# Kernel optimization log

Hardware: AMD Instinct MI355X
Metric: run time of the kernel (lower is better)

## Reference

```python
import jax, jax.numpy as jnp
import numpy as np

VOCAB, E, H, L, N = 32000, 256, 512, 512, 64


def setup_inputs() -> dict:
    key = jax.random.key(0)
    ks = jax.random.split(key, 8)
    s_in = 1.0 / np.sqrt(H + E)
    return {
        "x": jax.random.randint(ks[0], (L, N), 0, VOCAB),
        "emb": jax.random.normal(ks[1], (VOCAB, E), dtype=jnp.float32),
        # weights stored (in, out); math identical to torch Linear with W.T
        "Wz": jax.random.uniform(ks[2], (H + E, H), jnp.float32, -s_in, s_in),
        "bz": jax.random.uniform(ks[3], (H,), jnp.float32, -s_in, s_in),
        "Wr": jax.random.uniform(ks[4], (H + E, H), jnp.float32, -s_in, s_in),
        "br": jax.random.uniform(ks[5], (H,), jnp.float32, -s_in, s_in),
        "Wh": jax.random.uniform(ks[6], (H + E, H), jnp.float32, -s_in, s_in),
        "bh": jax.random.uniform(ks[7], (H,), jnp.float32, -s_in, s_in),
    }


def reference(x, emb, Wz, bz, Wr, br, Wh, bh):
    # x: (L, N) int indices -> embedded once: (L, N, E)
    xe = emb[x]
    h0 = jnp.zeros((x.shape[1], Wz.shape[1]), dtype=emb.dtype)

    def step(h, e_t):
        hx = jnp.concatenate([h, e_t], axis=1)            # (N, H+E)
        z = jax.nn.sigmoid(hx @ Wz + bz)                  # update gate
        r = jax.nn.sigmoid(hx @ Wr + br)                  # reset gate
        rhx = jnp.concatenate([r * h, e_t], axis=1)
        h_tilde = jnp.tanh(rhx @ Wh + bh)
        h_new = (1.0 - z) * h + z * h_tilde
        return h_new, h_new

    _, hs = jax.lax.scan(step, h0, xe)                    # hs: (L, N, H)
    return hs
```

## Files before the change

### kernel.cpp

```cpp
#include <hip/hip_runtime.h>


#define LSTEPS 512
#define NBATCH 64
#define HDIM   512
#define EDIM   256
#define KDIM   768
#define NBLK   32
#define TPB    256

typedef _Float16 f16x8 __attribute__((ext_vector_type(8)));
typedef float    f32x4 __attribute__((ext_vector_type(4)));
typedef unsigned long long u64;

__device__ __forceinline__ float sigm(float x){ return 1.0f/(1.0f+__expf(-x)); }
__device__ __forceinline__ float tanh_fast(float x){
  float e = __expf(2.0f*x);
  return 1.0f - 2.0f/(e + 1.0f);
}
__device__ __forceinline__ unsigned f16b(float x){
  union { _Float16 h; unsigned short u; } c; c.h = (_Float16)x; return (unsigned)c.u;
}

__global__ void prep_w(const float* __restrict__ Wz, const float* __restrict__ Wr,
                       const float* __restrict__ Wh, _Float16* __restrict__ wbuf){
  int tid = blockIdx.x*256 + threadIdx.x;
  int g   = tid / (HDIM*KDIM);
  int rem = tid - g*(HDIM*KDIM);
  int j   = rem / KDIM;
  int k   = rem - j*KDIM;
  const float* W = (g==0) ? Wz : ((g==1) ? Wr : Wh);
  wbuf[tid] = (_Float16)W[(size_t)k*HDIM + j];
}

__global__ void prep_emb(const int* __restrict__ x, const float* __restrict__ emb,
                         _Float16* __restrict__ ebuf){
  int tid = blockIdx.x*256 + threadIdx.x;
  int k4  = tid & 63;
  int tn  = tid >> 6;
  int row = x[tn];
  const float4 v = *(const float4*)(emb + (size_t)row*EDIM + (k4<<2));
  union { _Float16 h[4]; uint2 u; } p;
  p.h[0] = (_Float16)v.x; p.h[1] = (_Float16)v.y;
  p.h[2] = (_Float16)v.z; p.h[3] = (_Float16)v.w;
  *(uint2*)(ebuf + (size_t)tn*EDIM + (k4<<2)) = p.u;
}

__device__ __forceinline__ void store_x(_Float16* buf, int jc2, int n0, int lane,
                                        float v0, float v1, float v2, float v3){
  unsigned p01 = f16b(v0) | (f16b(v1) << 16);
  unsigned p23 = f16b(v2) | (f16b(v3) << 16);
  unsigned q01 = __shfl_xor(p01, 1, 64);
  unsigned q23 = __shfl_xor(p23, 1, 64);
  unsigned w0, w1; int r0;
  if (lane & 1){
    w0 = (q23 & 0xffffu) | (p23 << 16);
    w1 = (q23 >> 16)     | (p23 & 0xffff0000u);
    r0 = n0 + 2;
  } else {
    w0 = (p01 & 0xffffu) | (q01 << 16);
    w1 = (p01 >> 16)     | (q01 & 0xffff0000u);
    r0 = n0;
  }
  __hip_atomic_store((unsigned*)(buf + (size_t)r0*HDIM + jc2),     w0,
                     __ATOMIC_RELAXED, __HIP_MEMORY_SCOPE_AGENT);
  __hip_atomic_store((unsigned*)(buf + (size_t)(r0+1)*HDIM + jc2), w1,
                     __ATOMIC_RELAXED, __HIP_MEMORY_SCOPE_AGENT);
}

__device__ __forceinline__ void waitfl(unsigned* fl, unsigned target){
  const int l31 = threadIdx.x & 31;
  for (;;){
    unsigned v = __hip_atomic_load(&fl[l31], __ATOMIC_RELAXED, __HIP_MEMORY_SCOPE_AGENT);
    if (__all(v >= target)) break;
  }
}

__global__ __launch_bounds__(TPB, 1) void gru_persist(
    const _Float16* __restrict__ wbuf,
    const _Float16* __restrict__ ebuf,
    const float* __restrict__ bz, const float* __restrict__ br, const float* __restrict__ bh,
    _Float16* __restrict__ hx,
    _Float16* __restrict__ rhx,
    unsigned* __restrict__ hfl,
    unsigned* __restrict__ rhfl,
    float* __restrict__ out)
{
  __shared__ char wlds[3*16*1536];
  const int jbase = blockIdx.x * 16;

  for (int cidx = threadIdx.x; cidx < 3*16*96; cidx += TPB){
    int g   = cidx / (16*96);
    int rem = cidx - g*(16*96);
    int col = rem / 96;
    int kch = rem - col*96;
    const uint4 v = *(const uint4*)(wbuf + ((size_t)(g*HDIM + jbase + col))*KDIM + kch*8);
    int off = (((g*16 + col)*1536) + kch*16) ^ ((col & 7) << 4);
    *(uint4*)(wlds + off) = v;
  }
  __syncthreads();

  const int lane = threadIdx.x & 63;
  const int wave = threadIdx.x >> 6;
  const int c15  = lane & 15;
  const int kgrp = lane >> 4;
  const int jcol = jbase + c15;
  const int jc2  = jcol & ~1;
  const int arow = wave*16 + c15;
  const int n0   = wave*16 + kgrp*4;
  const int swz  = (c15 & 7) << 4;
  const int linz = ((      c15)*1536) + kgrp*16;
  const int linr = ((16  + c15)*1536) + kgrp*16;
  const int linh = ((32  + c15)*1536) + kgrp*16;
  const float bzj = bz[jcol];
  const float brj = br[jcol];
  const float bhj = bh[jcol];
  unsigned* myhfl  = hfl  + wave*32;
  unsigned* myrhfl = rhfl + wave*32;
  const u64* hrow  = (const u64*)hx  + (size_t)arow*128 + kgrp*2;
  const u64* rhrow = (const u64*)rhx + (size_t)arow*128 + kgrp*2;
  float hreg[4] = {0.f, 0.f, 0.f, 0.f};

  u64 q[32];

#define LOADX(BASE) do {                                                      \
    _Pragma("unroll")                                                         \
    for (int kc = 0; kc < 16; ++kc){                                          \
      q[2*kc]   = __hip_atomic_load((BASE) + kc*8,     __ATOMIC_RELAXED,      \
                                    __HIP_MEMORY_SCOPE_AGENT);                \
      q[2*kc+1] = __hip_atomic_load((BASE) + kc*8 + 1, __ATOMIC_RELAXED,      \
                                    __HIP_MEMORY_SCOPE_AGENT);                \
    }                                                                         \
  } while (0)

#define AFRAG(KC) ({ union { u64 d[2]; f16x8 v; } _a;                         \
                     _a.d[0] = q[2*(KC)]; _a.d[1] = q[2*(KC)+1]; _a.v; })

  for (int t = 0; t < LSTEPS; ++t){
    const _Float16* ae = ebuf + ((size_t)t*NBATCH + arow)*EDIM + kgrp*8;
    const unsigned tago = (unsigned)t;
    const unsigned tagn = (unsigned)(t + 1);

    f32x4 accr = {0.f,0.f,0.f,0.f};
    #pragma unroll
    for (int kc = 0; kc < 8; ++kc){
      f16x8 a   = *(const f16x8*)(ae + kc*32);
      f16x8 brv = *(const f16x8*)(wlds + ((linr + (16+kc)*64) ^ swz));
      accr = __builtin_amdgcn_mfma_f32_16x16x32_f16(a, brv, accr, 0, 0, 0);
    }
    waitfl(myhfl, tago);
    LOADX(hrow);
    #pragma unroll
    for (int kc = 0; kc < 16; ++kc){
      f16x8 brv = *(const f16x8*)(wlds + ((linr + kc*64) ^ swz));
      accr = __builtin_amdgcn_mfma_f32_16x16x32_f16(AFRAG(kc), brv, accr, 0, 0, 0);
    }
    float rh[4];
    #pragma unroll
    for (int i = 0; i < 4; ++i)
      rh[i] = sigm(accr[i] + brj) * hreg[i];
    store_x(rhx, jc2, n0, lane, rh[0], rh[1], rh[2], rh[3]);
    asm volatile("s_waitcnt vmcnt(0)" ::: "memory");
    if (lane == 0)
      __hip_atomic_store(&myrhfl[blockIdx.x], tagn,
                         __ATOMIC_RELAXED, __HIP_MEMORY_SCOPE_AGENT);

    f32x4 accz = {0.f,0.f,0.f,0.f};
    f32x4 acch = {0.f,0.f,0.f,0.f};
    #pragma unroll
    for (int kc = 0; kc < 16; ++kc){
      f16x8 bzv = *(const f16x8*)(wlds + ((linz + kc*64) ^ swz));
      accz = __builtin_amdgcn_mfma_f32_16x16x32_f16(AFRAG(kc), bzv, accz, 0, 0, 0);
    }
    #pragma unroll
    for (int kc = 0; kc < 8; ++kc){
      f16x8 a   = *(const f16x8*)(ae + kc*32);
      f16x8 bzv = *(const f16x8*)(wlds + ((linz + (16+kc)*64) ^ swz));
      f16x8 bhv = *(const f16x8*)(wlds + ((linh + (16+kc)*64) ^ swz));
      accz = __builtin_amdgcn_mfma_f32_16x16x32_f16(a, bzv, accz, 0, 0, 0);
      acch = __builtin_amdgcn_mfma_f32_16x16x32_f16(a, bhv, acch, 0, 0, 0);
    }
    float zreg[4];
    #pragma unroll
    for (int i = 0; i < 4; ++i) zreg[i] = sigm(accz[i] + bzj);

    waitfl(myrhfl, tagn);
    LOADX(rhrow);
    #pragma unroll
    for (int kc = 0; kc < 16; ++kc){
      f16x8 bhv = *(const f16x8*)(wlds + ((linh + kc*64) ^ swz));
      acch = __builtin_amdgcn_mfma_f32_16x16x32_f16(AFRAG(kc), bhv, acch, 0, 0, 0);
    }
    #pragma unroll
    for (int i = 0; i < 4; ++i){
      float ht = tanh_fast(acch[i] + bhj);
      float hn = hreg[i] + zreg[i]*(ht - hreg[i]);
      hreg[i] = hn;
      out[((size_t)t*NBATCH + (n0+i))*HDIM + jcol] = hn;
    }
    store_x(hx, jc2, n0, lane, hreg[0], hreg[1], hreg[2], hreg[3]);
    asm volatile("s_waitcnt vmcnt(0)" ::: "memory");
    if (lane == 0)
      __hip_atomic_store(&myhfl[blockIdx.x], tagn,
                         __ATOMIC_RELAXED, __HIP_MEMORY_SCOPE_AGENT);
  }
#undef LOADX
#undef AFRAG
}

extern "C" void kernel_launch(void* const* d_in, const int* in_sizes, int n_in,
                              void* d_out, int out_size, void* d_ws, size_t ws_size,
                              hipStream_t stream) {
  const int*   x   = (const int*)  d_in[0];
  const float* emb = (const float*)d_in[1];
  const float* Wz  = (const float*)d_in[2];
  const float* bz  = (const float*)d_in[3];
  const float* Wr  = (const float*)d_in[4];
  const float* br  = (const float*)d_in[5];
  const float* Wh  = (const float*)d_in[6];
  const float* bh  = (const float*)d_in[7];
  float* out = (float*)d_out;
  char*  ws  = (char*)d_ws;

  size_t off = 0;
  unsigned* hfl  = (unsigned*)(ws + off); off += 4*32*4;
  unsigned* rhfl = (unsigned*)(ws + off); off += 4*32*4;
  _Float16* hx   = (_Float16*)(ws + off); off += (size_t)NBATCH*HDIM*2;
  size_t zero_bytes = off;
  _Float16* rhx  = (_Float16*)(ws + off); off += (size_t)NBATCH*HDIM*2;
  _Float16* wbuf = (_Float16*)(ws + off); off += (size_t)3*HDIM*KDIM*2;
  _Float16* ebuf = (_Float16*)(ws + off); off += (size_t)LSTEPS*NBATCH*EDIM*2;

  hipMemsetAsync(ws, 0, zero_bytes, stream);

  prep_w  <<<(3*HDIM*KDIM)/256,          256, 0, stream>>>(Wz, Wr, Wh, wbuf);
  prep_emb<<<(LSTEPS*NBATCH*EDIM/4)/256, 256, 0, stream>>>(x, emb, ebuf);
  gru_persist<<<NBLK, TPB, 0, stream>>>(wbuf, ebuf, bz, br, bh,
                                        hx, rhx, hfl, rhfl, out);
}
```

Measured before the change: 5.413 ms.

## Replace per-block flag polling with atomic counters and prefetch embeddings

Swaps the per-block flag arrays, which were polled with a wave-wide 32-lane __all check, for one atomic counter per wave that each block increments and waiters poll with a single load. The embedding fragments for the next step are now loaded into registers after the h flag is signalled, taking those global loads off the critical path. The output store is moved after the signal so other blocks can proceed sooner. Atomic fetch_add on a shared counter adds contention on one cache line, and the wait target depends on all 32 blocks incrementing exactly once per step.

```diff
diff --git a/kernel.cpp b/kernel.cpp
--- a/kernel.cpp
+++ b/kernel.cpp
@@ -12,6 +12,8 @@
 typedef _Float16 f16x8 __attribute__((ext_vector_type(8)));
 typedef float    f32x4 __attribute__((ext_vector_type(4)));
 typedef unsigned long long u64;
+
+#define MFMA __builtin_amdgcn_mfma_f32_16x16x32_f16
 
 __device__ __forceinline__ float sigm(float x){ return 1.0f/(1.0f+__expf(-x)); }
 __device__ __forceinline__ float tanh_fast(float x){
@@ -68,11 +70,10 @@
                      __ATOMIC_RELAXED, __HIP_MEMORY_SCOPE_AGENT);
 }
 
-__device__ __forceinline__ void waitfl(unsigned* fl, unsigned target){
-  const int l31 = threadIdx.x & 31;
+__device__ __forceinline__ void waitcnt_ge(const unsigned* c, unsigned target){
   for (;;){
-    unsigned v = __hip_atomic_load(&fl[l31], __ATOMIC_RELAXED, __HIP_MEMORY_SCOPE_AGENT);
-    if (__all(v >= target)) break;
+    unsigned v = __hip_atomic_load(c, __ATOMIC_RELAXED, __HIP_MEMORY_SCOPE_AGENT);
+    if (v >= target) break;
   }
 }
 
@@ -82,8 +83,8 @@
     const float* __restrict__ bz, const float* __restrict__ br, const float* __restrict__ bh,
     _Float16* __restrict__ hx,
     _Float16* __restrict__ rhx,
-    unsigned* __restrict__ hfl,
-    unsigned* __restrict__ rhfl,
+    unsigned* __restrict__ cnth,
+    unsigned* __restrict__ cntrh,
     float* __restrict__ out)
 {
   __shared__ char wlds[3*16*1536];
@@ -115,13 +116,14 @@
   const float bzj = bz[jcol];
   const float brj = br[jcol];
   const float bhj = bh[jcol];
-  unsigned* myhfl  = hfl  + wave*32;
-  unsigned* myrhfl = rhfl + wave*32;
+  unsigned* mycnth  = cnth  + wave*32;
+  unsigned* mycntrh = cntrh + wave*32;
   const u64* hrow  = (const u64*)hx  + (size_t)arow*128 + kgrp*2;
   const u64* rhrow = (const u64*)rhx + (size_t)arow*128 + kgrp*2;
   float hreg[4] = {0.f, 0.f, 0.f, 0.f};
 
   u64 q[32];
+  f16x8 aereg[8];
 
 #define LOADX(BASE) do {                                                      \
     _Pragma("unroll")                                                         \
@@ -136,24 +138,28 @@
 #define AFRAG(KC) ({ union { u64 d[2]; f16x8 v; } _a;                         \
                      _a.d[0] = q[2*(KC)]; _a.d[1] = q[2*(KC)+1]; _a.v; })
 
+  {
+    const _Float16* ae0 = ebuf + (size_t)arow*EDIM + kgrp*8;
+    #pragma unroll
+    for (int kc = 0; kc < 8; ++kc) aereg[kc] = *(const f16x8*)(ae0 + kc*32);
+  }
+
   for (int t = 0; t < LSTEPS; ++t){
-    const _Float16* ae = ebuf + ((size_t)t*NBATCH + arow)*EDIM + kgrp*8;
-    const unsigned tago = (unsigned)t;
-    const unsigned tagn = (unsigned)(t + 1);
+    const unsigned tgt_h  = 32u*(unsigned)t;
+    const unsigned tgt_rh = 32u*(unsigned)(t + 1);
 
     f32x4 accr = {0.f,0.f,0.f,0.f};
     #pragma unroll
     for (int kc = 0; kc < 8; ++kc){
-      f16x8 a   = *(const f16x8*)(ae + kc*32);
       f16x8 brv = *(const f16x8*)(wlds + ((linr + (16+kc)*64) ^ swz));
-      accr = __builtin_amdgcn_mfma_f32_16x16x32_f16(a, brv, accr, 0, 0, 0);
-    }
-    waitfl(myhfl, tago);
+      accr = MFMA(aereg[kc], brv, accr, 0, 0, 0);
+    }
+    waitcnt_ge(mycnth, tgt_h);
     LOADX(hrow);
     #pragma unroll
     for (int kc = 0; kc < 16; ++kc){
       f16x8 brv = *(const f16x8*)(wlds + ((linr + kc*64) ^ swz));
-      accr = __builtin_amdgcn_mfma_f32_16x16x32_f16(AFRAG(kc), brv, accr, 0, 0, 0);
+      accr = MFMA(AFRAG(kc), brv, accr, 0, 0, 0);
     }
     float rh[4];
     #pragma unroll
@@ -161,48 +167,56 @@
       rh[i] = sigm(accr[i] + brj) * hreg[i];
     store_x(rhx, jc2, n0, lane, rh[0], rh[1], rh[2], rh[3]);
     asm volatile("s_waitcnt vmcnt(0)" ::: "memory");
+    __builtin_amdgcn_sched_barrier(0);
     if (lane == 0)
-      __hip_atomic_store(&myrhfl[blockIdx.x], tagn,
-                         __ATOMIC_RELAXED, __HIP_MEMORY_SCOPE_AGENT);
+      __hip_atomic_fetch_add(mycntrh, 1u,
+                             __ATOMIC_RELAXED, __HIP_MEMORY_SCOPE_AGENT);
 
     f32x4 accz = {0.f,0.f,0.f,0.f};
     f32x4 acch = {0.f,0.f,0.f,0.f};
     #pragma unroll
     for (int kc = 0; kc < 16; ++kc){
       f16x8 bzv = *(const f16x8*)(wlds + ((linz + kc*64) ^ swz));
-      accz = __builtin_amdgcn_mfma_f32_16x16x32_f16(AFRAG(kc), bzv, accz, 0, 0, 0);
+      accz = MFMA(AFRAG(kc), bzv, accz, 0, 0, 0);
     }
     #pragma unroll
     for (int kc = 0; kc < 8; ++kc){
-      f16x8 a   = *(const f16x8*)(ae + kc*32);
       f16x8 bzv = *(const f16x8*)(wlds + ((linz + (16+kc)*64) ^ swz));
       f16x8 bhv = *(const f16x8*)(wlds + ((linh + (16+kc)*64) ^ swz));
-      accz = __builtin_amdgcn_mfma_f32_16x16x32_f16(a, bzv, accz, 0, 0, 0);
-      acch = __builtin_amdgcn_mfma_f32_16x16x32_f16(a, bhv, acch, 0, 0, 0);
+      accz = MFMA(aereg[kc], bzv, accz, 0, 0, 0);
+      acch = MFMA(aereg[kc], bhv, acch, 0, 0, 0);
     }
     float zreg[4];
     #pragma unroll
     for (int i = 0; i < 4; ++i) zreg[i] = sigm(accz[i] + bzj);
 
-    waitfl(myrhfl, tagn);
+    waitcnt_ge(mycntrh, tgt_rh);
     LOADX(rhrow);
     #pragma unroll
     for (int kc = 0; kc < 16; ++kc){
       f16x8 bhv = *(const f16x8*)(wlds + ((linh + kc*64) ^ swz));
-      acch = __builtin_amdgcn_mfma_f32_16x16x32_f16(AFRAG(kc), bhv, acch, 0, 0, 0);
+      acch = MFMA(AFRAG(kc), bhv, acch, 0, 0, 0);
     }
     #pragma unroll
     for (int i = 0; i < 4; ++i){
       float ht = tanh_fast(acch[i] + bhj);
-      float hn = hreg[i] + zreg[i]*(ht - hreg[i]);
-      hreg[i] = hn;
-      out[((size_t)t*NBATCH + (n0+i))*HDIM + jcol] = hn;
+      hreg[i] = hreg[i] + zreg[i]*(ht - hreg[i]);
     }
     store_x(hx, jc2, n0, lane, hreg[0], hreg[1], hreg[2], hreg[3]);
     asm volatile("s_waitcnt vmcnt(0)" ::: "memory");
+    __builtin_amdgcn_sched_barrier(0);
     if (lane == 0)
-      __hip_atomic_store(&myhfl[blockIdx.x], tagn,
-                         __ATOMIC_RELAXED, __HIP_MEMORY_SCOPE_AGENT);
+      __hip_atomic_fetch_add(mycnth, 1u,
+                             __ATOMIC_RELAXED, __HIP_MEMORY_SCOPE_AGENT);
+
+    if (t + 1 < LSTEPS){
+      const _Float16* aen = ebuf + ((size_t)(t+1)*NBATCH + arow)*EDIM + kgrp*8;
+      #pragma unroll
+      for (int kc = 0; kc < 8; ++kc) aereg[kc] = *(const f16x8*)(aen + kc*32);
+    }
+    #pragma unroll
+    for (int i = 0; i < 4; ++i)
+      out[((size_t)t*NBATCH + (n0+i))*HDIM + jcol] = hreg[i];
   }
 #undef LOADX
 #undef AFRAG
@@ -223,18 +237,18 @@
   char*  ws  = (char*)d_ws;
 
   size_t off = 0;
-  unsigned* hfl  = (unsigned*)(ws + off); off += 4*32*4;
-  unsigned* rhfl = (unsigned*)(ws + off); off += 4*32*4;
-  _Float16* hx   = (_Float16*)(ws + off); off += (size_t)NBATCH*HDIM*2;
+  unsigned* cnth  = (unsigned*)(ws + off); off += 4*32*4;
+  unsigned* cntrh = (unsigned*)(ws + off); off += 4*32*4;
+  _Float16* hx    = (_Float16*)(ws + off); off += (size_t)NBATCH*HDIM*2;
   size_t zero_bytes = off;
-  _Float16* rhx  = (_Float16*)(ws + off); off += (size_t)NBATCH*HDIM*2;
-  _Float16* wbuf = (_Float16*)(ws + off); off += (size_t)3*HDIM*KDIM*2;
-  _Float16* ebuf = (_Float16*)(ws + off); off += (size_t)LSTEPS*NBATCH*EDIM*2;
+  _Float16* rhx   = (_Float16*)(ws + off); off += (size_t)NBATCH*HDIM*2;
+  _Float16* wbuf  = (_Float16*)(ws + off); off += (size_t)3*HDIM*KDIM*2;
+  _Float16* ebuf  = (_Float16*)(ws + off); off += (size_t)LSTEPS*NBATCH*EDIM*2;
 
   hipMemsetAsync(ws, 0, zero_bytes, stream);
 
   prep_w  <<<(3*HDIM*KDIM)/256,          256, 0, stream>>>(Wz, Wr, Wh, wbuf);
   prep_emb<<<(LSTEPS*NBATCH*EDIM/4)/256, 256, 0, stream>>>(x, emb, ebuf);
   gru_persist<<<NBLK, TPB, 0, stream>>>(wbuf, ebuf, bz, br, bh,
-                                        hx, rhx, hfl, rhfl, out);
-}
+                                        hx, rhx, cnth, cntrh, out);
+}
```

Measured after the change: 6.253 ms. +15.5%, slower.

## Halve persistent blocks to 16 with 32 columns each, prefetch embeddings, defer output stores

Applied to the files above, without the earlier changes.

The persistent GRU kernel now runs 16 blocks, each owning 32 hidden columns instead of 16. Each loaded h/rh fragment therefore feeds two MFMA chains, and the cross-block flag barrier polls 16 flags instead of 32. The next step's embedding fragments are prefetched into registers while the z/h gate matmuls run. The output stores are moved after the h flag is published, so they sit off the critical path. The cost is double the LDS footprint (144KB), more registers, and fewer CUs doing the per-step matmul work.

```diff
diff --git a/kernel.cpp b/kernel.cpp
--- a/kernel.cpp
+++ b/kernel.cpp
@@ -6,12 +6,15 @@
 #define HDIM   512
 #define EDIM   256
 #define KDIM   768
-#define NBLK   32
+#define NBLK   16
+#define COLS   32
 #define TPB    256
 
 typedef _Float16 f16x8 __attribute__((ext_vector_type(8)));
 typedef float    f32x4 __attribute__((ext_vector_type(4)));
 typedef unsigned long long u64;
+
+#define MFMA __builtin_amdgcn_mfma_f32_16x16x32_f16
 
 __device__ __forceinline__ float sigm(float x){ return 1.0f/(1.0f+__expf(-x)); }
 __device__ __forceinline__ float tanh_fast(float x){
@@ -20,6 +23,9 @@
 }
 __device__ __forceinline__ unsigned f16b(float x){
   union { _Float16 h; unsigned short u; } c; c.h = (_Float16)x; return (unsigned)c.u;
+}
+__device__ __forceinline__ f16x8 AFU(u64 a, u64 b){
+  union { u64 d[2]; f16x8 v; } c; c.d[0] = a; c.d[1] = b; return c.v;
 }
 
 __global__ void prep_w(const float* __restrict__ Wz, const float* __restrict__ Wr,
@@ -68,10 +74,11 @@
                      __ATOMIC_RELAXED, __HIP_MEMORY_SCOPE_AGENT);
 }
 
-__device__ __forceinline__ void waitfl(unsigned* fl, unsigned target){
-  const int l31 = threadIdx.x & 31;
+__device__ __forceinline__ void waitfl(const unsigned* fl, unsigned target){
+  const int l15 = threadIdx.x & 15;
   for (;;){
-    unsigned v = __hip_atomic_load(&fl[l31], __ATOMIC_RELAXED, __HIP_MEMORY_SCOPE_AGENT);
+    unsigned v = __hip_atomic_load(&fl[l15], __ATOMIC_RELAXED,
+                                   __HIP_MEMORY_SCOPE_AGENT);
     if (__all(v >= target)) break;
   }
 }
@@ -83,19 +90,19 @@
     _Float16* __restrict__ hx,
     _Float16* __restrict__ rhx,
     unsigned* __restrict__ hfl,
-    unsigned* __restrict__ rhfl,
+    unsigned* __restrict__ rfl,
     float* __restrict__ out)
 {
-  __shared__ char wlds[3*16*1536];
-  const int jbase = blockIdx.x * 16;
-
-  for (int cidx = threadIdx.x; cidx < 3*16*96; cidx += TPB){
-    int g   = cidx / (16*96);
-    int rem = cidx - g*(16*96);
+  __shared__ char wlds[3*COLS*1536];
+  const int jbase = blockIdx.x * COLS;
+
+  for (int cidx = threadIdx.x; cidx < 3*COLS*96; cidx += TPB){
+    int g   = cidx / (COLS*96);
+    int rem = cidx - g*(COLS*96);
     int col = rem / 96;
     int kch = rem - col*96;
     const uint4 v = *(const uint4*)(wbuf + ((size_t)(g*HDIM + jbase + col))*KDIM + kch*8);
-    int off = (((g*16 + col)*1536) + kch*16) ^ ((col & 7) << 4);
+    int off = (((g*COLS + col)*1536) + kch*16) ^ ((col & 7) << 4);
     *(uint4*)(wlds + off) = v;
   }
   __syncthreads();
@@ -104,24 +111,30 @@
   const int wave = threadIdx.x >> 6;
   const int c15  = lane & 15;
   const int kgrp = lane >> 4;
-  const int jcol = jbase + c15;
-  const int jc2  = jcol & ~1;
   const int arow = wave*16 + c15;
   const int n0   = wave*16 + kgrp*4;
   const int swz  = (c15 & 7) << 4;
-  const int linz = ((      c15)*1536) + kgrp*16;
-  const int linr = ((16  + c15)*1536) + kgrp*16;
-  const int linh = ((32  + c15)*1536) + kgrp*16;
-  const float bzj = bz[jcol];
-  const float brj = br[jcol];
-  const float bhj = bh[jcol];
-  unsigned* myhfl  = hfl  + wave*32;
-  unsigned* myrhfl = rhfl + wave*32;
-  const u64* hrow  = (const u64*)hx  + (size_t)arow*128 + kgrp*2;
-  const u64* rhrow = (const u64*)rhx + (size_t)arow*128 + kgrp*2;
-  float hreg[4] = {0.f, 0.f, 0.f, 0.f};
+  const int jcol0 = jbase + c15;
+  const int jcol1 = jbase + 16 + c15;
+  const int jc20  = jcol0 & ~1;
+  const int jc21  = jcol1 & ~1;
+  const int lz0 = ((0*COLS + c15     )*1536) + kgrp*16;
+  const int lz1 = ((0*COLS + c15 + 16)*1536) + kgrp*16;
+  const int lr0 = ((1*COLS + c15     )*1536) + kgrp*16;
+  const int lr1 = ((1*COLS + c15 + 16)*1536) + kgrp*16;
+  const int lh0 = ((2*COLS + c15     )*1536) + kgrp*16;
+  const int lh1 = ((2*COLS + c15 + 16)*1536) + kgrp*16;
+  const float bzj0 = bz[jcol0], bzj1 = bz[jcol1];
+  const float brj0 = br[jcol0], brj1 = br[jcol1];
+  const float bhj0 = bh[jcol0], bhj1 = bh[jcol1];
+  unsigned* myhfl = hfl + wave*NBLK;
+  unsigned* myrfl = rfl + wave*NBLK;
+  const u64* hrow = (const u64*)hx  + (size_t)arow*128 + kgrp*2;
+  const u64* rrow = (const u64*)rhx + (size_t)arow*128 + kgrp*2;
+  float hreg0[4] = {0,0,0,0}, hreg1[4] = {0,0,0,0};
 
   u64 q[32];
+  f16x8 aeA[8], aeB[8];
 
 #define LOADX(BASE) do {                                                      \
     _Pragma("unroll")                                                         \
@@ -133,79 +146,117 @@
     }                                                                         \
   } while (0)
 
-#define AFRAG(KC) ({ union { u64 d[2]; f16x8 v; } _a;                         \
-                     _a.d[0] = q[2*(KC)]; _a.d[1] = q[2*(KC)+1]; _a.v; })
+  {
+    const _Float16* ae0 = ebuf + (size_t)arow*EDIM + kgrp*8;
+    #pragma unroll
+    for (int kc = 0; kc < 8; ++kc) aeA[kc] = *(const f16x8*)(ae0 + kc*32);
+  }
 
   for (int t = 0; t < LSTEPS; ++t){
-    const _Float16* ae = ebuf + ((size_t)t*NBATCH + arow)*EDIM + kgrp*8;
-    const unsigned tago = (unsigned)t;
     const unsigned tagn = (unsigned)(t + 1);
 
-    f32x4 accr = {0.f,0.f,0.f,0.f};
+    f32x4 accr0 = {0,0,0,0}, accr1 = {0,0,0,0};
     #pragma unroll
     for (int kc = 0; kc < 8; ++kc){
-      f16x8 a   = *(const f16x8*)(ae + kc*32);
-      f16x8 brv = *(const f16x8*)(wlds + ((linr + (16+kc)*64) ^ swz));
-      accr = __builtin_amdgcn_mfma_f32_16x16x32_f16(a, brv, accr, 0, 0, 0);
-    }
-    waitfl(myhfl, tago);
+      f16x8 b0 = *(const f16x8*)(wlds + ((lr0 + (16+kc)*64) ^ swz));
+      f16x8 b1 = *(const f16x8*)(wlds + ((lr1 + (16+kc)*64) ^ swz));
+      accr0 = MFMA(aeA[kc], b0, accr0, 0, 0, 0);
+      accr1 = MFMA(aeA[kc], b1, accr1, 0, 0, 0);
+    }
+    waitfl(myhfl, (unsigned)t);
     LOADX(hrow);
     #pragma unroll
     for (int kc = 0; kc < 16; ++kc){
-      f16x8 brv = *(const f16x8*)(wlds + ((linr + kc*64) ^ swz));
-      accr = __builtin_amdgcn_mfma_f32_16x16x32_f16(AFRAG(kc), brv, accr, 0, 0, 0);
-    }
-    float rh[4];
-    #pragma unroll
-    for (int i = 0; i < 4; ++i)
-      rh[i] = sigm(accr[i] + brj) * hreg[i];
-    store_x(rhx, jc2, n0, lane, rh[0], rh[1], rh[2], rh[3]);
+      f16x8 a  = AFU(q[2*kc], q[2*kc+1]);
+      f16x8 b0 = *(const f16x8*)(wlds + ((lr0 + kc*64) ^ swz));
+      f16x8 b1 = *(const f16x8*)(wlds + ((lr1 + kc*64) ^ swz));
+      accr0 = MFMA(a, b0, accr0, 0, 0, 0);
+      accr1 = MFMA(a, b1, accr1, 0, 0, 0);
+    }
+    float rh0[4], rh1[4];
+    #pragma unroll
+    for (int i = 0; i < 4; ++i){
+      rh0[i] = sigm(accr0[i] + brj0) * hreg0[i];
+      rh1[i] = sigm(accr1[i] + brj1) * hreg1[i];
+    }
+    store_x(rhx, jc20, n0, lane, rh0[0], rh0[1], rh0[2], rh0[3]);
+    store_x(rhx, jc21, n0, lane, rh1[0], rh1[1], rh1[2], rh1[3]);
     asm volatile("s_waitcnt vmcnt(0)" ::: "memory");
+    __builtin_amdgcn_sched_barrier(0);
     if (lane == 0)
-      __hip_atomic_store(&myrhfl[blockIdx.x], tagn,
+      __hip_atomic_store(&myrfl[blockIdx.x], tagn,
                          __ATOMIC_RELAXED, __HIP_MEMORY_SCOPE_AGENT);
 
-    f32x4 accz = {0.f,0.f,0.f,0.f};
-    f32x4 acch = {0.f,0.f,0.f,0.f};
+    {
+      const int tn = (t + 1 < LSTEPS) ? (t + 1) : t;
+      const _Float16* aen = ebuf + ((size_t)tn*NBATCH + arow)*EDIM + kgrp*8;
+      #pragma unroll
+      for (int kc = 0; kc < 8; ++kc) aeB[kc] = *(const f16x8*)(aen + kc*32);
+    }
+
+    f32x4 accz0 = {0,0,0,0}, accz1 = {0,0,0,0};
+    f32x4 acch0 = {0,0,0,0}, acch1 = {0,0,0,0};
     #pragma unroll
     for (int kc = 0; kc < 16; ++kc){
-      f16x8 bzv = *(const f16x8*)(wlds + ((linz + kc*64) ^ swz));
-      accz = __builtin_amdgcn_mfma_f32_16x16x32_f16(AFRAG(kc), bzv, accz, 0, 0, 0);
+      f16x8 a  = AFU(q[2*kc], q[2*kc+1]);
+      f16x8 b0 = *(const f16x8*)(wlds + ((lz0 + kc*64) ^ swz));
+      f16x8 b1 = *(const f16x8*)(wlds + ((lz1 + kc*64) ^ swz));
+      accz0 = MFMA(a, b0, accz0, 0, 0, 0);
+      accz1 = MFMA(a, b1, accz1, 0, 0, 0);
     }
     #pragma unroll
     for (int kc = 0; kc < 8; ++kc){
-      f16x8 a   = *(const f16x8*)(ae + kc*32);
-      f16x8 bzv = *(const f16x8*)(wlds + ((linz + (16+kc)*64) ^ swz));
-      f16x8 bhv = *(const f16x8*)(wlds + ((linh + (16+kc)*64) ^ swz));
-      accz = __builtin_amdgcn_mfma_f32_16x16x32_f16(a, bzv, accz, 0, 0, 0);
-      acch = __builtin_amdgcn_mfma_f32_16x16x32_f16(a, bhv, acch, 0, 0, 0);
-    }
-    float zreg[4];
-    #pragma unroll
-    for (int i = 0; i < 4; ++i) zreg[i] = sigm(accz[i] + bzj);
-
-    waitfl(myrhfl, tagn);
-    LOADX(rhrow);
+      f16x8 z0 = *(const f16x8*)(wlds + ((lz0 + (16+kc)*64) ^ swz));
+      f16x8 z1 = *(const f16x8*)(wlds + ((lz1 + (16+kc)*64) ^ swz));
+      f16x8 h0 = *(const f16x8*)(wlds + ((lh0 + (16+kc)*64) ^ swz));
+      f16x8 h1 = *(const f16x8*)(wlds + ((lh1 + (16+kc)*64) ^ swz));
+      accz0 = MFMA(aeA[kc], z0, accz0, 0, 0, 0);
+      accz1 = MFMA(aeA[kc], z1, accz1, 0, 0, 0);
+      acch0 = MFMA(aeA[kc], h0, acch0, 0, 0, 0);
+      acch1 = MFMA(aeA[kc], h1, acch1, 0, 0, 0);
+    }
+    float zreg0[4], zreg1[4];
+    #pragma unroll
+    for (int i = 0; i < 4; ++i){
+      zreg0[i] = sigm(accz0[i] + bzj0);
+      zreg1[i] = sigm(accz1[i] + bzj1);
+    }
+
+    waitfl(myrfl, tagn);
+    LOADX(rrow);
     #pragma unroll
     for (int kc = 0; kc < 16; ++kc){
-      f16x8 bhv = *(const f16x8*)(wlds + ((linh + kc*64) ^ swz));
-      acch = __builtin_amdgcn_mfma_f32_16x16x32_f16(AFRAG(kc), bhv, acch, 0, 0, 0);
-    }
-    #pragma unroll
-    for (int i = 0; i < 4; ++i){
-      float ht = tanh_fast(acch[i] + bhj);
-      float hn = hreg[i] + zreg[i]*(ht - hreg[i]);
-      hreg[i] = hn;
-      out[((size_t)t*NBATCH + (n0+i))*HDIM + jcol] = hn;
-    }
-    store_x(hx, jc2, n0, lane, hreg[0], hreg[1], hreg[2], hreg[3]);
+      f16x8 a  = AFU(q[2*kc], q[2*kc+1]);
+      f16x8 b0 = *(const f16x8*)(wlds + ((lh0 + kc*64) ^ swz));
+      f16x8 b1 = *(const f16x8*)(wlds + ((lh1 + kc*64) ^ swz));
+      acch0 = MFMA(a, b0, acch0, 0, 0, 0);
+      acch1 = MFMA(a, b1, acch1, 0, 0, 0);
+    }
+    #pragma unroll
+    for (int i = 0; i < 4; ++i){
+      float ht0 = tanh_fast(acch0[i] + bhj0);
+      float ht1 = tanh_fast(acch1[i] + bhj1);
+      hreg0[i] = hreg0[i] + zreg0[i]*(ht0 - hreg0[i]);
+      hreg1[i] = hreg1[i] + zreg1[i]*(ht1 - hreg1[i]);
+    }
+    store_x(hx, jc20, n0, lane, hreg0[0], hreg0[1], hreg0[2], hreg0[3]);
+    store_x(hx, jc21, n0, lane, hreg1[0], hreg1[1], hreg1[2], hreg1[3]);
     asm volatile("s_waitcnt vmcnt(0)" ::: "memory");
+    __builtin_amdgcn_sched_barrier(0);
     if (lane == 0)
       __hip_atomic_store(&myhfl[blockIdx.x], tagn,
                          __ATOMIC_RELAXED, __HIP_MEMORY_SCOPE_AGENT);
+
+    #pragma unroll
+    for (int i = 0; i < 4; ++i){
+      int n = n0 + i;
+      out[((size_t)t*NBATCH + n)*HDIM + jcol0] = hreg0[i];
+      out[((size_t)t*NBATCH + n)*HDIM + jcol1] = hreg1[i];
+    }
+    #pragma unroll
+    for (int kc = 0; kc < 8; ++kc) aeA[kc] = aeB[kc];
   }
 #undef LOADX
-#undef AFRAG
 }
 
 extern "C" void kernel_launch(void* const* d_in, const int* in_sizes, int n_in,
@@ -223,8 +274,8 @@
   char*  ws  = (char*)d_ws;
 
   size_t off = 0;
-  unsigned* hfl  = (unsigned*)(ws + off); off += 4*32*4;
-  unsigned* rhfl = (unsigned*)(ws + off); off += 4*32*4;
+  unsigned* hfl  = (unsigned*)(ws + off); off += 4*NBLK*4;
+  unsigned* rfl  = (unsigned*)(ws + off); off += 4*NBLK*4;
   _Float16* hx   = (_Float16*)(ws + off); off += (size_t)NBATCH*HDIM*2;
   size_t zero_bytes = off;
   _Float16* rhx  = (_Float16*)(ws + off); off += (size_t)NBATCH*HDIM*2;
@@ -236,5 +287,5 @@
   prep_w  <<<(3*HDIM*KDIM)/256,          256, 0, stream>>>(Wz, Wr, Wh, wbuf);
   prep_emb<<<(LSTEPS*NBATCH*EDIM/4)/256, 256, 0, stream>>>(x, emb, ebuf);
   gru_persist<<<NBLK, TPB, 0, stream>>>(wbuf, ebuf, bz, br, bh,
-                                        hx, rhx, hfl, rhfl, out);
-}
+                                        hx, rhx, hfl, rfl, out);
+}
```

Measured after the change: 5.746 ms. 6.2% more time.
